# Performance work log

Hardware: AMD Instinct MI355X
Metric: run time of the kernel (lower is better)

## Reference

```python
import jax, jax.numpy as jnp
import numpy as np

N = 100000      # nodes
E = 1600000     # edges (avg degree 16)
F_IN = 512      # nfeat
C = 64          # nclass


def setup_inputs() -> dict:
    key = jax.random.key(0)
    k1, k2, k3 = jax.random.split(key, 3)
    x = jax.random.normal(k1, (N, F_IN), dtype=jnp.float32)
    edge_index = jax.random.randint(k2, (2, E), 0, N, dtype=jnp.int32)
    # GCNConv weight (glorot-ish) and bias
    W = jax.random.normal(k3, (F_IN, C), dtype=jnp.float32) * (1.0 / np.sqrt(F_IN))
    b = jnp.zeros((C,), dtype=jnp.float32)
    return {"x": x, "W": W, "b": b, "edge_index": edge_index}


def reference(x, W, b, edge_index):
    # Standard GCNConv (sheaf_laplacian=None): project, add self-loops,
    # symmetric normalization D^{-1/2}(A+I)D^{-1/2}, aggregate, bias.
    h = x @ W  # [N, C] project first (C < F_IN), as torch_geometric does
    self_loops = jnp.arange(N, dtype=edge_index.dtype)
    src = jnp.concatenate([edge_index[0], self_loops])
    dst = jnp.concatenate([edge_index[1], self_loops])
    deg = jax.ops.segment_sum(jnp.ones_like(dst, dtype=h.dtype), dst, num_segments=N)
    dinv = jnp.where(deg > 0, jax.lax.rsqrt(deg), 0.0)  # deg^{-1/2}
    norm = dinv[src] * dinv[dst]  # [E+N]
    msgs = h[src] * norm[:, None]  # gather + scale, [E+N, C]
    out = jax.ops.segment_sum(msgs, dst, num_segments=N) + b  # [N, C]
    return jax.nn.log_softmax(out, axis=1)
```

## Files before the change

kernel.cpp:

```cpp
#include <hip/hip_runtime.h>
#include <hip/hip_bf16.h>

#define F_IN 512
#define NCLS 64
#define SCAN_BLK 512

typedef __attribute__((ext_vector_type(8))) short short8;
typedef __attribute__((ext_vector_type(4))) float f32x4;

static __device__ __forceinline__ short bf16_of(float f) {
    __hip_bfloat16 h = __float2bfloat16(f);
    short s;
    __builtin_memcpy(&s, &h, 2);
    return s;
}
static __device__ __forceinline__ float b2f(short s) {
    unsigned u = ((unsigned)(unsigned short)s) << 16;
    float f;
    __builtin_memcpy(&f, &u, 4);
    return f;
}

__global__ void zero_cnt(int* __restrict__ cnt, int n) {
    int i = blockIdx.x * blockDim.x + threadIdx.x;
    if (i < n) cnt[i] = 0;
}

__global__ void deg_count(const int* __restrict__ dst, int* __restrict__ cnt,
                          int* __restrict__ rank, int e) {
    int i = blockIdx.x * blockDim.x + threadIdx.x;
    if (i < e) rank[i] = atomicAdd(&cnt[dst[i]], 1);
}

__global__ __launch_bounds__(SCAN_BLK) void scan1(const int* __restrict__ cnt,
                                                  int* __restrict__ off,
                                                  int* __restrict__ partials,
                                                  float* __restrict__ dinv, int n) {
    __shared__ int s[SCAN_BLK];
    int tid = threadIdx.x;
    int i = blockIdx.x * SCAN_BLK + tid;
    int v = (i < n) ? cnt[i] : 0;
    if (i < n) dinv[i] = rsqrtf(1.0f + (float)v);
    s[tid] = v;
    __syncthreads();
#pragma unroll
    for (int d = 1; d < SCAN_BLK; d <<= 1) {
        int t = (tid >= d) ? s[tid - d] : 0;
        __syncthreads();
        s[tid] += t;
        __syncthreads();
    }
    if (i < n) off[i] = s[tid] - v;
    if (tid == SCAN_BLK - 1) partials[blockIdx.x] = s[tid];
}

__global__ __launch_bounds__(256) void scan2(int* __restrict__ partials, int p) {
    __shared__ int s[256];
    int tid = threadIdx.x;
    int v = (tid < p) ? partials[tid] : 0;
    s[tid] = v;
    __syncthreads();
#pragma unroll
    for (int d = 1; d < 256; d <<= 1) {
        int t = (tid >= d) ? s[tid - d] : 0;
        __syncthreads();
        s[tid] += t;
        __syncthreads();
    }
    if (tid < p) partials[tid] = s[tid] - v;
}

__global__ void scan3(int* __restrict__ off, const int* __restrict__ partials,
                      int n, int e) {
    int i = blockIdx.x * blockDim.x + threadIdx.x;
    if (i < n) off[i] += partials[i / SCAN_BLK];
    if (i == 0) off[n] = e;
}

__global__ void fill_csr(const int* __restrict__ src, const int* __restrict__ dst,
                         const int* __restrict__ off, const int* __restrict__ rank,
                         int* __restrict__ eidx, int e) {
    int i = blockIdx.x * blockDim.x + threadIdx.x;
    if (i < e) eidx[off[dst[i]] + rank[i]] = src[i];
}

__global__ void wconvert(const float* __restrict__ W, short* __restrict__ Wb) {
    int t = blockIdx.x * blockDim.x + threadIdx.x;
    if (t >= 4096) return;
    int c = t >> 10;
    int kk = (t >> 6) & 15;
    int l = t & 63;
    short8 v;
#pragma unroll
    for (int j = 0; j < 8; ++j) {
        v[j] = bf16_of(W[(size_t)(kk * 32 + (l >> 4) * 8 + j) * NCLS + c * 16 + (l & 15)]);
    }
    reinterpret_cast<short8*>(Wb)[t] = v;
}

__global__ __launch_bounds__(256) void gemm_mfma(const float* __restrict__ x,
                                                 const short* __restrict__ Wb,
                                                 const float* __restrict__ dinv,
                                                 short* __restrict__ g, int n) {
    const int wave = threadIdx.x >> 6;
    const int lane = threadIdx.x & 63;
    const int rowTile = blockIdx.x * 64 + wave * 16;

    int arow = rowTile + (lane & 15);
    if (arow > n - 1) arow = n - 1;
    const float* xr = x + (size_t)arow * F_IN + ((lane >> 4) * 8);

    const short8* wb8 = reinterpret_cast<const short8*>(Wb);

    f32x4 acc0 = {0.f, 0.f, 0.f, 0.f};
    f32x4 acc1 = {0.f, 0.f, 0.f, 0.f};
    f32x4 acc2 = {0.f, 0.f, 0.f, 0.f};
    f32x4 acc3 = {0.f, 0.f, 0.f, 0.f};

#pragma unroll 4
    for (int kk = 0; kk < 16; ++kk) {
        float4 f0 = *reinterpret_cast<const float4*>(xr + kk * 32);
        float4 f1 = *reinterpret_cast<const float4*>(xr + kk * 32 + 4);
        short8 a;
        a[0] = bf16_of(f0.x); a[1] = bf16_of(f0.y);
        a[2] = bf16_of(f0.z); a[3] = bf16_of(f0.w);
        a[4] = bf16_of(f1.x); a[5] = bf16_of(f1.y);
        a[6] = bf16_of(f1.z); a[7] = bf16_of(f1.w);
        short8 b0 = wb8[(0 * 16 + kk) * 64 + lane];
        short8 b1 = wb8[(1 * 16 + kk) * 64 + lane];
        short8 b2 = wb8[(2 * 16 + kk) * 64 + lane];
        short8 b3 = wb8[(3 * 16 + kk) * 64 + lane];
        acc0 = __builtin_amdgcn_mfma_f32_16x16x32_bf16(a, b0, acc0, 0, 0, 0);
        acc1 = __builtin_amdgcn_mfma_f32_16x16x32_bf16(a, b1, acc1, 0, 0, 0);
        acc2 = __builtin_amdgcn_mfma_f32_16x16x32_bf16(a, b2, acc2, 0, 0, 0);
        acc3 = __builtin_amdgcn_mfma_f32_16x16x32_bf16(a, b3, acc3, 0, 0, 0);
    }

    const int col = lane & 15;
    const int rbase = rowTile + (lane >> 4) * 4;
#pragma unroll
    for (int j = 0; j < 4; ++j) {
        int r = rbase + j;
        if (r < n) {
            float dv = dinv[r];
            short* go = g + (size_t)r * NCLS + col;
            go[0]  = bf16_of(acc0[j] * dv);
            go[16] = bf16_of(acc1[j] * dv);
            go[32] = bf16_of(acc2[j] * dv);
            go[48] = bf16_of(acc3[j] * dv);
        }
    }
}

__global__ __launch_bounds__(256) void aggregate(const short* __restrict__ g,
                                                 const float* __restrict__ dinv,
                                                 const float* __restrict__ b,
                                                 const int* __restrict__ off,
                                                 const int* __restrict__ eidx,
                                                 float* __restrict__ out, int n) {
    const int wave = threadIdx.x >> 6;
    const int lane = threadIdx.x & 63;
    const int grp = lane >> 3;
    const int li = lane & 7;
    const int node = (blockIdx.x * 4 + wave) * 8 + grp;
    if (node >= n) return;

    const int s0 = off[node];
    const int s1 = off[node + 1];

    const short8* g8 = reinterpret_cast<const short8*>(g);

    float acc[8];
    {
        short8 v = g8[(size_t)node * 8 + li];
#pragma unroll
        for (int c = 0; c < 8; ++c) acc[c] = b2f(v[c]);
    }

    int t = s0;
    for (; t + 4 <= s1; t += 4) {
        int sa = eidx[t];
        int sb = eidx[t + 1];
        int sc = eidx[t + 2];
        int sd = eidx[t + 3];
        short8 va = g8[(size_t)sa * 8 + li];
        short8 vb = g8[(size_t)sb * 8 + li];
        short8 vc = g8[(size_t)sc * 8 + li];
        short8 vd = g8[(size_t)sd * 8 + li];
#pragma unroll
        for (int c = 0; c < 8; ++c)
            acc[c] += (b2f(va[c]) + b2f(vb[c])) + (b2f(vc[c]) + b2f(vd[c]));
    }
    for (; t < s1; ++t) {
        int sa = eidx[t];
        short8 va = g8[(size_t)sa * 8 + li];
#pragma unroll
        for (int c = 0; c < 8; ++c) acc[c] += b2f(va[c]);
    }

    const float dn = dinv[node];
    const float4 b0 = reinterpret_cast<const float4*>(b)[li * 2];
    const float4 b1 = reinterpret_cast<const float4*>(b)[li * 2 + 1];
    float v[8];
    v[0] = acc[0] * dn + b0.x; v[1] = acc[1] * dn + b0.y;
    v[2] = acc[2] * dn + b0.z; v[3] = acc[3] * dn + b0.w;
    v[4] = acc[4] * dn + b1.x; v[5] = acc[5] * dn + b1.y;
    v[6] = acc[6] * dn + b1.z; v[7] = acc[7] * dn + b1.w;

    float m = v[0];
#pragma unroll
    for (int c = 1; c < 8; ++c) m = fmaxf(m, v[c]);
#pragma unroll
    for (int o = 1; o < 8; o <<= 1) m = fmaxf(m, __shfl_xor(m, o));

    float ex = 0.f;
#pragma unroll
    for (int c = 0; c < 8; ++c) ex += __expf(v[c] - m);
#pragma unroll
    for (int o = 1; o < 8; o <<= 1) ex += __shfl_xor(ex, o);
    const float lg = m + __logf(ex);

    float4 r0, r1;
    r0.x = v[0] - lg; r0.y = v[1] - lg; r0.z = v[2] - lg; r0.w = v[3] - lg;
    r1.x = v[4] - lg; r1.y = v[5] - lg; r1.z = v[6] - lg; r1.w = v[7] - lg;
    float4* o4 = reinterpret_cast<float4*>(out + (size_t)node * NCLS);
    o4[li * 2] = r0;
    o4[li * 2 + 1] = r1;
}

extern "C" void kernel_launch(void* const* d_in, const int* in_sizes, int n_in,
                              void* d_out, int out_size, void* d_ws, size_t ws_size,
                              hipStream_t stream) {
    const float* x = (const float*)d_in[0];
    const float* W = (const float*)d_in[1];
    const float* b = (const float*)d_in[2];
    const int* edge_index = (const int*)d_in[3];

    const int N = in_sizes[0] / F_IN;
    const int E = in_sizes[3] / 2;
    const int* src = edge_index;
    const int* dst = edge_index + E;

    float* out = (float*)d_out;

    char* ws = (char*)d_ws;
    short* g      = (short*)ws;  ws += (size_t)N * NCLS * 2;
    short* Wb     = (short*)ws;  ws += 4096 * 16;
    float* dinv   = (float*)ws;  ws += (size_t)N * 4;
    int*   cnt    = (int*)ws;    ws += (size_t)N * 4;
    int*   off    = (int*)ws;    ws += (size_t)(N + 4) * 4;
    int*   parts  = (int*)ws;    ws += 1024 * 4;
    int*   rank   = (int*)ws;    ws += (size_t)E * 4;
    int*   eidx   = (int*)ws;

    const int nScanBlocks = (N + SCAN_BLK - 1) / SCAN_BLK;

    zero_cnt<<<(N + 255) / 256, 256, 0, stream>>>(cnt, N);

    deg_count<<<(E + 255) / 256, 256, 0, stream>>>(dst, cnt, rank, E);

    scan1<<<nScanBlocks, SCAN_BLK, 0, stream>>>(cnt, off, parts, dinv, N);
    scan2<<<1, 256, 0, stream>>>(parts, nScanBlocks);
    scan3<<<(N + 255) / 256, 256, 0, stream>>>(off, parts, N, E);

    fill_csr<<<(E + 255) / 256, 256, 0, stream>>>(src, dst, off, rank, eidx, E);

    wconvert<<<16, 256, 0, stream>>>(W, Wb);

    gemm_mfma<<<(N + 63) / 64, 256, 0, stream>>>(x, Wb, dinv, g, N);

    aggregate<<<(N + 31) / 32, 256, 0, stream>>>(g, dinv, b, off, eidx, out, N);
}
```

Before: 189.6 us.

## Co-schedule GEMM with degree counting and drop scan3 by deferring offsets

Merges the weight conversion with count zeroing, and runs the MFMA projection and the atomic degree count as interleaved roles of one launch, so the compute-bound GEMM overlaps the atomic-bound counting. The source-side dinv scale moves from the GEMM epilogue into the aggregation, which lets the GEMM run before degrees are known. The scan3 pass is removed by adding block partials wherever offsets are read. Ranks are stored as 16-bit values and edges are processed four per thread with vector loads. This adds a dinv gather per edge and assumes no node's in-degree exceeds 65535.

```diff
diff --git a/kernel.cpp b/kernel.cpp
--- a/kernel.cpp
+++ b/kernel.cpp
@@ -21,90 +21,61 @@
     return f;
 }
 
-__global__ void zero_cnt(int* __restrict__ cnt, int n) {
-    int i = blockIdx.x * blockDim.x + threadIdx.x;
-    if (i < n) cnt[i] = 0;
-}
-
-__global__ void deg_count(const int* __restrict__ dst, int* __restrict__ cnt,
-                          int* __restrict__ rank, int e) {
-    int i = blockIdx.x * blockDim.x + threadIdx.x;
-    if (i < e) rank[i] = atomicAdd(&cnt[dst[i]], 1);
-}
-
-__global__ __launch_bounds__(SCAN_BLK) void scan1(const int* __restrict__ cnt,
-                                                  int* __restrict__ off,
-                                                  int* __restrict__ partials,
-                                                  float* __restrict__ dinv, int n) {
-    __shared__ int s[SCAN_BLK];
-    int tid = threadIdx.x;
-    int i = blockIdx.x * SCAN_BLK + tid;
-    int v = (i < n) ? cnt[i] : 0;
-    if (i < n) dinv[i] = rsqrtf(1.0f + (float)v);
-    s[tid] = v;
-    __syncthreads();
-#pragma unroll
-    for (int d = 1; d < SCAN_BLK; d <<= 1) {
-        int t = (tid >= d) ? s[tid - d] : 0;
-        __syncthreads();
-        s[tid] += t;
-        __syncthreads();
-    }
-    if (i < n) off[i] = s[tid] - v;
-    if (tid == SCAN_BLK - 1) partials[blockIdx.x] = s[tid];
-}
-
-__global__ __launch_bounds__(256) void scan2(int* __restrict__ partials, int p) {
-    __shared__ int s[256];
-    int tid = threadIdx.x;
-    int v = (tid < p) ? partials[tid] : 0;
-    s[tid] = v;
-    __syncthreads();
-#pragma unroll
-    for (int d = 1; d < 256; d <<= 1) {
-        int t = (tid >= d) ? s[tid - d] : 0;
-        __syncthreads();
-        s[tid] += t;
-        __syncthreads();
-    }
-    if (tid < p) partials[tid] = s[tid] - v;
-}
-
-__global__ void scan3(int* __restrict__ off, const int* __restrict__ partials,
-                      int n, int e) {
-    int i = blockIdx.x * blockDim.x + threadIdx.x;
-    if (i < n) off[i] += partials[i / SCAN_BLK];
-    if (i == 0) off[n] = e;
-}
-
-__global__ void fill_csr(const int* __restrict__ src, const int* __restrict__ dst,
-                         const int* __restrict__ off, const int* __restrict__ rank,
-                         int* __restrict__ eidx, int e) {
-    int i = blockIdx.x * blockDim.x + threadIdx.x;
-    if (i < e) eidx[off[dst[i]] + rank[i]] = src[i];
-}
-
-__global__ void wconvert(const float* __restrict__ W, short* __restrict__ Wb) {
-    int t = blockIdx.x * blockDim.x + threadIdx.x;
-    if (t >= 4096) return;
-    int c = t >> 10;
-    int kk = (t >> 6) & 15;
-    int l = t & 63;
-    short8 v;
-#pragma unroll
-    for (int j = 0; j < 8; ++j) {
-        v[j] = bf16_of(W[(size_t)(kk * 32 + (l >> 4) * 8 + j) * NCLS + c * 16 + (l & 15)]);
-    }
-    reinterpret_cast<short8*>(Wb)[t] = v;
-}
-
-__global__ __launch_bounds__(256) void gemm_mfma(const float* __restrict__ x,
-                                                 const short* __restrict__ Wb,
-                                                 const float* __restrict__ dinv,
-                                                 short* __restrict__ g, int n) {
+__global__ __launch_bounds__(256) void prelude(const float* __restrict__ W,
+                                               short* __restrict__ Wb,
+                                               int* __restrict__ cnt, int n) {
+    const int bid = blockIdx.x;
+    if (bid < 16) {
+        int t = bid * 256 + threadIdx.x;
+        int c = t >> 10;
+        int kk = (t >> 6) & 15;
+        int l = t & 63;
+        short8 v;
+#pragma unroll
+        for (int j = 0; j < 8; ++j) {
+            v[j] = bf16_of(W[(size_t)(kk * 32 + (l >> 4) * 8 + j) * NCLS + c * 16 + (l & 15)]);
+        }
+        reinterpret_cast<short8*>(Wb)[t] = v;
+    } else {
+        int i = (bid - 16) * 256 + threadIdx.x;
+        if (i < n) cnt[i] = 0;
+    }
+}
+
+__global__ __launch_bounds__(256) void megaA(const float* __restrict__ x,
+                                             const short* __restrict__ Wb,
+                                             short* __restrict__ g, int n,
+                                             const int* __restrict__ dst,
+                                             int* __restrict__ cnt,
+                                             unsigned short* __restrict__ rank, int e,
+                                             int gemmBlocks, int degBlocks) {
+    const int bid = blockIdx.x;
+    const int m2 = 2 * (gemmBlocks < degBlocks ? gemmBlocks : degBlocks);
+    int role, idx;
+    if (bid < m2) { role = bid & 1; idx = bid >> 1; }
+    else if (gemmBlocks > degBlocks) { role = 0; idx = bid - degBlocks; }
+    else { role = 1; idx = bid - gemmBlocks; }
+
+    if (role == 1) {
+        int base = (idx * 256 + threadIdx.x) * 4;
+        if (base + 4 <= e) {
+            int4 d4 = *reinterpret_cast<const int4*>(dst + base);
+            ushort4 r;
+            r.x = (unsigned short)atomicAdd(&cnt[d4.x], 1);
+            r.y = (unsigned short)atomicAdd(&cnt[d4.y], 1);
+            r.z = (unsigned short)atomicAdd(&cnt[d4.z], 1);
+            r.w = (unsigned short)atomicAdd(&cnt[d4.w], 1);
+            *reinterpret_cast<ushort4*>(rank + base) = r;
+        } else {
+            for (int i = base; i < e; ++i)
+                rank[i] = (unsigned short)atomicAdd(&cnt[dst[i]], 1);
+        }
+        return;
+    }
+
     const int wave = threadIdx.x >> 6;
     const int lane = threadIdx.x & 63;
-    const int rowTile = blockIdx.x * 64 + wave * 16;
+    const int rowTile = idx * 64 + wave * 16;
 
     int arow = rowTile + (lane & 15);
     if (arow > n - 1) arow = n - 1;
@@ -142,13 +113,72 @@
     for (int j = 0; j < 4; ++j) {
         int r = rbase + j;
         if (r < n) {
-            float dv = dinv[r];
             short* go = g + (size_t)r * NCLS + col;
-            go[0]  = bf16_of(acc0[j] * dv);
-            go[16] = bf16_of(acc1[j] * dv);
-            go[32] = bf16_of(acc2[j] * dv);
-            go[48] = bf16_of(acc3[j] * dv);
+            go[0]  = bf16_of(acc0[j]);
+            go[16] = bf16_of(acc1[j]);
+            go[32] = bf16_of(acc2[j]);
+            go[48] = bf16_of(acc3[j]);
         }
+    }
+}
+
+__global__ __launch_bounds__(SCAN_BLK) void scan1(const int* __restrict__ cnt,
+                                                  int* __restrict__ off,
+                                                  int* __restrict__ partials,
+                                                  float* __restrict__ dinv, int n) {
+    __shared__ int s[SCAN_BLK];
+    int tid = threadIdx.x;
+    int i = blockIdx.x * SCAN_BLK + tid;
+    int v = (i < n) ? cnt[i] : 0;
+    if (i < n) dinv[i] = rsqrtf(1.0f + (float)v);
+    s[tid] = v;
+    __syncthreads();
+#pragma unroll
+    for (int d = 1; d < SCAN_BLK; d <<= 1) {
+        int t = (tid >= d) ? s[tid - d] : 0;
+        __syncthreads();
+        s[tid] += t;
+        __syncthreads();
+    }
+    if (i < n) off[i] = s[tid] - v;
+    if (i == n - 1) off[n] = s[tid];
+    if (tid == SCAN_BLK - 1) partials[blockIdx.x] = s[tid];
+}
+
+__global__ __launch_bounds__(256) void scan2(int* __restrict__ partials, int p) {
+    __shared__ int s[256];
+    int tid = threadIdx.x;
+    int v = (tid < p) ? partials[tid] : 0;
+    s[tid] = v;
+    __syncthreads();
+#pragma unroll
+    for (int d = 1; d < 256; d <<= 1) {
+        int t = (tid >= d) ? s[tid - d] : 0;
+        __syncthreads();
+        s[tid] += t;
+        __syncthreads();
+    }
+    if (tid < p) partials[tid] = s[tid] - v;
+}
+
+__global__ __launch_bounds__(256) void fill_csr(const int* __restrict__ src,
+                                                const int* __restrict__ dst,
+                                                const int* __restrict__ off,
+                                                const int* __restrict__ parts,
+                                                const unsigned short* __restrict__ rank,
+                                                int* __restrict__ eidx, int e) {
+    int base = (blockIdx.x * 256 + threadIdx.x) * 4;
+    if (base + 4 <= e) {
+        int4 s4 = *reinterpret_cast<const int4*>(src + base);
+        int4 d4 = *reinterpret_cast<const int4*>(dst + base);
+        ushort4 r4 = *reinterpret_cast<const ushort4*>(rank + base);
+        eidx[off[d4.x] + parts[d4.x >> 9] + r4.x] = s4.x;
+        eidx[off[d4.y] + parts[d4.y >> 9] + r4.y] = s4.y;
+        eidx[off[d4.z] + parts[d4.z >> 9] + r4.z] = s4.z;
+        eidx[off[d4.w] + parts[d4.w >> 9] + r4.w] = s4.w;
+    } else {
+        for (int i = base; i < e; ++i)
+            eidx[off[dst[i]] + parts[dst[i] >> 9] + rank[i]] = src[i];
     }
 }
 
@@ -156,6 +186,7 @@
                                                  const float* __restrict__ dinv,
                                                  const float* __restrict__ b,
                                                  const int* __restrict__ off,
+                                                 const int* __restrict__ parts,
                                                  const int* __restrict__ eidx,
                                                  float* __restrict__ out, int n) {
     const int wave = threadIdx.x >> 6;
@@ -165,16 +196,18 @@
     const int node = (blockIdx.x * 4 + wave) * 8 + grp;
     if (node >= n) return;
 
-    const int s0 = off[node];
-    const int s1 = off[node + 1];
+    const int s0 = off[node] + parts[node >> 9];
+    const int np1 = node + 1;
+    const int s1 = off[np1] + parts[(np1 == n ? n - 1 : np1) >> 9];
 
     const short8* g8 = reinterpret_cast<const short8*>(g);
+    const float dn = dinv[node];
 
     float acc[8];
     {
         short8 v = g8[(size_t)node * 8 + li];
 #pragma unroll
-        for (int c = 0; c < 8; ++c) acc[c] = b2f(v[c]);
+        for (int c = 0; c < 8; ++c) acc[c] = b2f(v[c]) * dn;
     }
 
     int t = s0;
@@ -183,22 +216,23 @@
         int sb = eidx[t + 1];
         int sc = eidx[t + 2];
         int sd = eidx[t + 3];
+        float da = dinv[sa], db = dinv[sb], dc = dinv[sc], dd = dinv[sd];
         short8 va = g8[(size_t)sa * 8 + li];
         short8 vb = g8[(size_t)sb * 8 + li];
         short8 vc = g8[(size_t)sc * 8 + li];
         short8 vd = g8[(size_t)sd * 8 + li];
 #pragma unroll
         for (int c = 0; c < 8; ++c)
-            acc[c] += (b2f(va[c]) + b2f(vb[c])) + (b2f(vc[c]) + b2f(vd[c]));
+            acc[c] += (b2f(va[c]) * da + b2f(vb[c]) * db) + (b2f(vc[c]) * dc + b2f(vd[c]) * dd);
     }
     for (; t < s1; ++t) {
         int sa = eidx[t];
+        float da = dinv[sa];
         short8 va = g8[(size_t)sa * 8 + li];
 #pragma unroll
-        for (int c = 0; c < 8; ++c) acc[c] += b2f(va[c]);
-    }
-
-    const float dn = dinv[node];
+        for (int c = 0; c < 8; ++c) acc[c] += b2f(va[c]) * da;
+    }
+
     const float4 b0 = reinterpret_cast<const float4*>(b)[li * 2];
     const float4 b1 = reinterpret_cast<const float4*>(b)[li * 2 + 1];
     float v[8];
@@ -244,30 +278,28 @@
     float* out = (float*)d_out;
 
     char* ws = (char*)d_ws;
-    short* g      = (short*)ws;  ws += (size_t)N * NCLS * 2;
-    short* Wb     = (short*)ws;  ws += 4096 * 16;
-    float* dinv   = (float*)ws;  ws += (size_t)N * 4;
-    int*   cnt    = (int*)ws;    ws += (size_t)N * 4;
-    int*   off    = (int*)ws;    ws += (size_t)(N + 4) * 4;
-    int*   parts  = (int*)ws;    ws += 1024 * 4;
-    int*   rank   = (int*)ws;    ws += (size_t)E * 4;
-    int*   eidx   = (int*)ws;
+    short* g     = (short*)ws;  ws += (size_t)N * NCLS * 2;
+    short* Wb    = (short*)ws;  ws += 4096 * 16;
+    float* dinv  = (float*)ws;  ws += (size_t)N * 4;
+    int*   cnt   = (int*)ws;    ws += (size_t)N * 4;
+    int*   off   = (int*)ws;    ws += (size_t)(N + 4) * 4;
+    int*   parts = (int*)ws;    ws += 1024 * 4;
+    unsigned short* rank = (unsigned short*)ws;  ws += (size_t)((E + 7) & ~7) * 2;
+    int*   eidx  = (int*)ws;
 
     const int nScanBlocks = (N + SCAN_BLK - 1) / SCAN_BLK;
-
-    zero_cnt<<<(N + 255) / 256, 256, 0, stream>>>(cnt, N);
-
-    deg_count<<<(E + 255) / 256, 256, 0, stream>>>(dst, cnt, rank, E);
+    const int gemmBlocks = (N + 63) / 64;
+    const int degBlocks = (E + 1023) / 1024;
+
+    prelude<<<16 + (N + 255) / 256, 256, 0, stream>>>(W, Wb, cnt, N);
+
+    megaA<<<gemmBlocks + degBlocks, 256, 0, stream>>>(x, Wb, g, N, dst, cnt, rank, E,
+                                                      gemmBlocks, degBlocks);
 
     scan1<<<nScanBlocks, SCAN_BLK, 0, stream>>>(cnt, off, parts, dinv, N);
     scan2<<<1, 256, 0, stream>>>(parts, nScanBlocks);
-    scan3<<<(N + 255) / 256, 256, 0, stream>>>(off, parts, N, E);
-
-    fill_csr<<<(E + 255) / 256, 256, 0, stream>>>(src, dst, off, rank, eidx, E);
-
-    wconvert<<<16, 256, 0, stream>>>(W, Wb);
-
-    gemm_mfma<<<(N + 63) / 64, 256, 0, stream>>>(x, Wb, dinv, g, N);
-
-    aggregate<<<(N + 31) / 32, 256, 0, stream>>>(g, dinv, b, off, eidx, out, N);
-}
+
+    fill_csr<<<degBlocks, 256, 0, stream>>>(src, dst, off, parts, rank, eidx, E);
+
+    aggregate<<<(N + 31) / 32, 256, 0, stream>>>(g, dinv, b, off, parts, eidx, out, N);
+}
```

Result: no change. 186.5 us (-1.6%).
